# Performance work log

Hardware: AMD Instinct MI355X
Metric: run time of the kernel (lower is better)

The kernel has to match this reference:

```python
import jax, jax.numpy as jnp
import numpy as np

B, L, D, H, NL, V, W = 4, 2048, 512, 8, 4, 258, 8
HD = D // H


def setup_inputs() -> dict:
    key = jax.random.key(0)
    ks = jax.random.split(key, 12)
    s = 0.02
    x = jax.random.randint(ks[0], (B, L), 0, V, dtype=jnp.int32)
    patch_lengths = jnp.full((B, 256), W, dtype=jnp.int32)  # sum over patches == L
    emb = jax.random.normal(ks[1], (V, D), jnp.float32) * s
    ent_w = jax.random.normal(ks[2], (D, 1), jnp.float32) * s
    ent_b = jnp.zeros((D,), jnp.float32)
    qkv_w = jax.random.normal(ks[3], (NL, 3 * D, D), jnp.float32) * s
    qkv_b = jnp.zeros((NL, 3 * D), jnp.float32)
    ao_w = jax.random.normal(ks[4], (NL, D, D), jnp.float32) * s
    ao_b = jnp.zeros((NL, D), jnp.float32)
    ln1_s = jnp.ones((NL, D), jnp.float32)
    ln1_b = jnp.zeros((NL, D), jnp.float32)
    ln2_s = jnp.ones((NL, D), jnp.float32)
    ln2_b = jnp.zeros((NL, D), jnp.float32)
    ff1_w = jax.random.normal(ks[5], (NL, 4 * D, D), jnp.float32) * s
    ff1_b = jnp.zeros((NL, 4 * D), jnp.float32)
    ff2_w = jax.random.normal(ks[6], (NL, D, 4 * D), jnp.float32) * s
    ff2_b = jnp.zeros((NL, D), jnp.float32)
    out_w = jax.random.normal(ks[7], (V, D), jnp.float32) * s
    return {"emb": emb, "ent_w": ent_w, "ent_b": ent_b, "qkv_w": qkv_w,
            "qkv_b": qkv_b, "ao_w": ao_w, "ao_b": ao_b, "ln1_s": ln1_s,
            "ln1_b": ln1_b, "ln2_s": ln2_s, "ln2_b": ln2_b, "ff1_w": ff1_w,
            "ff1_b": ff1_b, "ff2_w": ff2_w, "ff2_b": ff2_b, "out_w": out_w,
            "x": x, "patch_lengths": patch_lengths}


def _layernorm(h, scale, bias, eps=1e-5):
    mu = jnp.mean(h, axis=-1, keepdims=True)
    var = jnp.mean(jnp.square(h - mu), axis=-1, keepdims=True)
    return (h - mu) * jax.lax.rsqrt(var + eps) * scale + bias


def _entropy_features(x, dtype):
    # fused sliding-window histogram via one-hot cumsum (replaces per-window bincount loop)
    onehot = jax.nn.one_hot(x, 256, dtype=dtype)            # [B, L, 256]
    c = jnp.cumsum(onehot, axis=1)
    cpad = jnp.concatenate([jnp.zeros_like(c[:, :1]), c], axis=1)
    counts = cpad[:, W:] - cpad[:, :-W]                     # [B, L-W+1, 256]
    p = counts / W
    ent = -jnp.sum(p * jnp.log2(p + 1e-10), axis=-1)        # zero-count terms contribute exactly 0
    full = jnp.zeros(x.shape, dtype).at[:, :x.shape[1] - W + 1].set(ent)
    return full[..., None]                                  # [B, L, 1]


def _block(h, p):
    qkv_w, qkv_b, ao_w, ao_b, l1s, l1b, l2s, l2b, f1w, f1b, f2w, f2b = p
    g = _layernorm(h, l1s, l1b)
    qkv = g @ qkv_w.T + qkv_b                                # [B, L, 3D]
    q, k, v = jnp.split(qkv, 3, axis=-1)
    q = q.reshape(B, L, H, HD)
    k = k.reshape(B, L, H, HD)
    v = v.reshape(B, L, H, HD)
    scores = jnp.einsum('blhd,bmhd->bhlm', q, k) / np.sqrt(HD).astype(h.dtype)
    attn = jax.nn.softmax(scores, axis=-1)
    o = jnp.einsum('bhlm,bmhd->blhd', attn, v).reshape(B, L, D)
    h = h + o @ ao_w.T + ao_b
    g = _layernorm(h, l2s, l2b)
    g = jax.nn.gelu(g @ f1w.T + f1b, approximate=False) @ f2w.T + f2b
    return h + g, None


def reference(emb, ent_w, ent_b, qkv_w, qkv_b, ao_w, ao_b, ln1_s, ln1_b,
              ln2_s, ln2_b, ff1_w, ff1_b, ff2_w, ff2_b, out_w, x, patch_lengths):
    tok = emb[x]                                             # [B, L, D]
    ent = _entropy_features(x, tok.dtype)                    # [B, L, 1]
    ent_emb = ent * ent_w[:, 0] + ent_b                      # Linear(1, D)
    h = tok + ent_emb
    h, _ = jax.lax.scan(_block, h,
                        (qkv_w, qkv_b, ao_w, ao_b, ln1_s, ln1_b,
                         ln2_s, ln2_b, ff1_w, ff1_b, ff2_w, ff2_b))
    # NOTE: the original module's global_transformer/patch-pool branch does not
    # feed the returned logits (dead code); logits come from the local stream h.
    logits = h @ out_w.T                                     # [B, L, V]
    return logits
```

## Files before the change

### kernel.cpp

```cpp
#include <hip/hip_runtime.h>
#include <hip/hip_bf16.h>
#include <math.h>

#define BB 4
#define LL 2048
#define DD 512
#define HH 8
#define NLAYER 4
#define VV 258
#define WW 8
#define HDIM 64
#define MM (BB * LL)
#define VPAD 384

#define C8 0.18033688f

typedef __attribute__((ext_vector_type(8))) short short8v;
typedef __attribute__((ext_vector_type(4))) float float4v;

typedef __attribute__((address_space(3))) unsigned int lds_u32;
typedef const __attribute__((address_space(1))) unsigned int glb_u32;

__device__ __forceinline__ unsigned short f2bf(float x) {
    unsigned int u = __float_as_uint(x);
    unsigned int r = (u + 0x7fffu + ((u >> 16) & 1u)) >> 16;
    return (unsigned short)r;
}
__device__ __forceinline__ float bf2f(unsigned short u) {
    return __uint_as_float((unsigned)u << 16);
}

__device__ __forceinline__ unsigned lds_addr(const void* p) {
    return (unsigned)(size_t)(__attribute__((address_space(3))) const void*)p;
}

#define E0 (NLAYER * 3 * DD * DD)
#define E1 (E0 + NLAYER * DD * DD)
#define E2 (E1 + NLAYER * 4 * DD * DD)
#define E3 (E2 + NLAYER * 4 * DD * DD)
#define E4 (E3 + VPAD * DD)

__global__ __launch_bounds__(256)
void cvt_all_kernel(const float* __restrict__ qkv_w, const float* __restrict__ ao_w,
                    const float* __restrict__ ff1_w, const float* __restrict__ ff2_w,
                    const float* __restrict__ out_w, unsigned short* __restrict__ dst)
{
    int i = (blockIdx.x * 256 + threadIdx.x) * 4;
    float4 v;
    if (i < E0)      v = *reinterpret_cast<const float4*>(qkv_w + i);
    else if (i < E1) v = *reinterpret_cast<const float4*>(ao_w + (i - E0));
    else if (i < E2) v = *reinterpret_cast<const float4*>(ff1_w + (i - E1));
    else if (i < E3) v = *reinterpret_cast<const float4*>(ff2_w + (i - E2));
    else {
        int idx = i - E3;
        if ((idx >> 9) < VV) v = *reinterpret_cast<const float4*>(out_w + idx);
        else                 v = (float4){0.f, 0.f, 0.f, 0.f};
    }
    uint2 pk;
    pk.x = (unsigned)f2bf(v.x) | ((unsigned)f2bf(v.y) << 16);
    pk.y = (unsigned)f2bf(v.z) | ((unsigned)f2bf(v.w) << 16);
    *reinterpret_cast<uint2*>(dst + i) = pk;
}

__global__ __launch_bounds__(256)
void embed_ln_kernel(const int* __restrict__ x,
                     const float* __restrict__ emb,
                     const float* __restrict__ ent_w,
                     const float* __restrict__ ent_b,
                     const float* __restrict__ ln_s,
                     const float* __restrict__ ln_b,
                     unsigned short* __restrict__ h,
                     unsigned short* __restrict__ g)
{
    int w = threadIdx.x >> 6, lane = threadIdx.x & 63;
    int row = blockIdx.x * 4 + w;
    int b = row / LL, l = row % LL;

    float ent = 0.f;
    if (l <= LL - WW) {
        int win[WW];
        #pragma unroll
        for (int i = 0; i < WW; i++) win[i] = x[b * LL + l + i];
        float s = 0.f;
        #pragma unroll
        for (int i = 0; i < WW; i++) {
            if (win[i] < 256) {
                int c = 0;
                #pragma unroll
                for (int j = 0; j < WW; j++) c += (win[j] == win[i]) ? 1 : 0;
                s += log2f((float)c * 0.125f + 1e-10f);
            }
        }
        ent = -s * 0.125f;
    }

    int tok = x[row];
    const float* erow = emb + (size_t)tok * DD + lane * 8;
    float v[8], ew[8], eb[8];
    *reinterpret_cast<float4*>(v)      = *reinterpret_cast<const float4*>(erow);
    *reinterpret_cast<float4*>(v + 4)  = *reinterpret_cast<const float4*>(erow + 4);
    *reinterpret_cast<float4*>(ew)     = *reinterpret_cast<const float4*>(ent_w + lane * 8);
    *reinterpret_cast<float4*>(ew + 4) = *reinterpret_cast<const float4*>(ent_w + lane * 8 + 4);
    *reinterpret_cast<float4*>(eb)     = *reinterpret_cast<const float4*>(ent_b + lane * 8);
    *reinterpret_cast<float4*>(eb + 4) = *reinterpret_cast<const float4*>(ent_b + lane * 8 + 4);

    float sum = 0.f, sq = 0.f;
    #pragma unroll
    for (int i = 0; i < 8; i++) {
        v[i] = v[i] + ent * ew[i] + eb[i];
        sum += v[i]; sq += v[i] * v[i];
    }
    unsigned int hpk[4];
    #pragma unroll
    for (int i = 0; i < 4; i++)
        hpk[i] = (unsigned)f2bf(v[2*i]) | ((unsigned)f2bf(v[2*i+1]) << 16);
    *reinterpret_cast<uint4*>(h + (size_t)row * DD + lane * 8) =
        *reinterpret_cast<const uint4*>(hpk);

    #pragma unroll
    for (int off = 32; off > 0; off >>= 1) {
        sum += __shfl_xor(sum, off);
        sq  += __shfl_xor(sq, off);
    }
    float mu = sum * (1.f / DD);
    float var = sq * (1.f / DD) - mu * mu;
    float rstd = rsqrtf(var + 1e-5f);

    float s8[8], bi[8];
    *reinterpret_cast<float4*>(s8)     = *reinterpret_cast<const float4*>(ln_s + lane * 8);
    *reinterpret_cast<float4*>(s8 + 4) = *reinterpret_cast<const float4*>(ln_s + lane * 8 + 4);
    *reinterpret_cast<float4*>(bi)     = *reinterpret_cast<const float4*>(ln_b + lane * 8);
    *reinterpret_cast<float4*>(bi + 4) = *reinterpret_cast<const float4*>(ln_b + lane * 8 + 4);

    unsigned int pk[4];
    #pragma unroll
    for (int i = 0; i < 4; i++) {
        unsigned short lo = f2bf((v[2*i]   - mu) * rstd * s8[2*i]   + bi[2*i]);
        unsigned short hi = f2bf((v[2*i+1] - mu) * rstd * s8[2*i+1] + bi[2*i+1]);
        pk[i] = (unsigned)lo | ((unsigned)hi << 16);
    }
    *reinterpret_cast<uint4*>(g + (size_t)row * DD + lane * 8) =
        *reinterpret_cast<const uint4*>(pk);
}

__global__ __launch_bounds__(256)
void ln_kernel(const unsigned short* __restrict__ h,
               const float* __restrict__ scale,
               const float* __restrict__ bias,
               unsigned short* __restrict__ g)
{
    int w = threadIdx.x >> 6, lane = threadIdx.x & 63;
    int row = blockIdx.x * 4 + w;

    uint4 raw = *reinterpret_cast<const uint4*>(h + (size_t)row * DD + lane * 8);
    const unsigned* rw = reinterpret_cast<const unsigned*>(&raw);
    float v[8];
    #pragma unroll
    for (int i = 0; i < 4; i++) {
        v[2*i]   = __uint_as_float(rw[i] << 16);
        v[2*i+1] = __uint_as_float(rw[i] & 0xffff0000u);
    }

    float sum = 0.f, sq = 0.f;
    #pragma unroll
    for (int i = 0; i < 8; i++) { sum += v[i]; sq += v[i] * v[i]; }
    #pragma unroll
    for (int off = 32; off > 0; off >>= 1) {
        sum += __shfl_xor(sum, off);
        sq  += __shfl_xor(sq, off);
    }
    float mu = sum * (1.f / DD);
    float var = sq * (1.f / DD) - mu * mu;
    float rstd = rsqrtf(var + 1e-5f);

    float s[8], bi[8];
    *reinterpret_cast<float4*>(s)      = *reinterpret_cast<const float4*>(scale + lane * 8);
    *reinterpret_cast<float4*>(s + 4)  = *reinterpret_cast<const float4*>(scale + lane * 8 + 4);
    *reinterpret_cast<float4*>(bi)     = *reinterpret_cast<const float4*>(bias + lane * 8);
    *reinterpret_cast<float4*>(bi + 4) = *reinterpret_cast<const float4*>(bias + lane * 8 + 4);

    unsigned int pk[4];
    #pragma unroll
    for (int i = 0; i < 4; i++) {
        unsigned short lo = f2bf((v[2*i]   - mu) * rstd * s[2*i]   + bi[2*i]);
        unsigned short hi = f2bf((v[2*i+1] - mu) * rstd * s[2*i+1] + bi[2*i+1]);
        pk[i] = (unsigned)lo | ((unsigned)hi << 16);
    }
    *reinterpret_cast<uint4*>(g + (size_t)row * DD + lane * 8) =
        *reinterpret_cast<const uint4*>(pk);
}

template<bool HAS_BIAS, bool GELU, bool RESID, bool QSCALE, int OMODE, int MT>
__global__ __launch_bounds__(MT * 2)
void gemm_mfma(const unsigned short* __restrict__ A,
               const unsigned short* __restrict__ W,
               const float* __restrict__ bias,
               const unsigned short* __restrict__ resid,
               void* __restrict__ Cv,
               int Nn, int Kk)
{
    constexpr int NW = MT / 32;
    constexpr int BLOADS = 512 / MT;
    constexpr int VMN = 4 + BLOADS;

    __shared__ unsigned short As[2][MT * 64];
    __shared__ unsigned short Bs[2][128 * 64];

    int t = threadIdx.x;
    int w = t >> 6, lane = t & 63;
    int wr = (MT == 128) ? (w >> 1) : 0;
    int wc = (MT == 128) ? (w & 1) : w;
    int l15 = lane & 15, l4 = lane >> 4;
    int m0 = blockIdx.y * MT, n0 = blockIdx.x * 128;

    int lrow = lane >> 3;
    int segp = (lane & 7) ^ lrow;

    float4v acc[4][4];
    #pragma unroll
    for (int i = 0; i < 4; i++)
        #pragma unroll
        for (int j = 0; j < 4; j++)
            acc[i][j] = (float4v){0.f, 0.f, 0.f, 0.f};

    #define STAGE(buf, k0) do {                                                   \
        _Pragma("unroll")                                                         \
        for (int i_ = 0; i_ < 4; i_++) {                                          \
            int r_ = i_ * (NW * 8) + w * 8 + lrow;                                \
            __builtin_amdgcn_global_load_lds(                                     \
                (glb_u32*)(A + (size_t)(m0 + r_) * Kk + (k0) + segp * 8),         \
                (lds_u32*)(As[buf] + i_ * (NW * 512) + w * 512), 16, 0, 0);       \
        }                                                                         \
        _Pragma("unroll")                                                         \
        for (int i_ = 0; i_ < BLOADS; i_++) {                                     \
            int r_ = i_ * (NW * 8) + w * 8 + lrow;                                \
            __builtin_amdgcn_global_load_lds(                                     \
                (glb_u32*)(W + (size_t)(n0 + r_) * Kk + (k0) + segp * 8),         \
                (lds_u32*)(Bs[buf] + i_ * (NW * 512) + w * 512), 16, 0, 0);       \
        } } while (0)

    int nk = Kk >> 6;
    STAGE(0, 0);
    for (int kt = 0; kt < nk; kt++) {
        int cur = kt & 1;
        if (kt + 1 < nk) {
            STAGE(cur ^ 1, (kt + 1) << 6);
            __builtin_amdgcn_sched_barrier(0);
            if constexpr (VMN == 8)  asm volatile("s_waitcnt vmcnt(8)");
            else                     asm volatile("s_waitcnt vmcnt(12)");
            __builtin_amdgcn_sched_barrier(0);
        } else {
            __builtin_amdgcn_sched_barrier(0);
            asm volatile("s_waitcnt vmcnt(0)");
            __builtin_amdgcn_sched_barrier(0);
        }
        __builtin_amdgcn_s_barrier();

        const char* asb = (const char*)As[cur];
        const char* bsb = (const char*)Bs[cur];
        #pragma unroll
        for (int kc = 0; kc < 2; kc++) {
            short8v af[4], bfr[4];
            #pragma unroll
            for (int mf = 0; mf < 4; mf++) {
                int row = wr * 64 + mf * 16 + l15;
                int off = (row * 128 + kc * 64 + l4 * 16) ^ ((row & 7) << 4);
                af[mf] = *reinterpret_cast<const short8v*>(asb + off);
            }
            #pragma unroll
            for (int nf = 0; nf < 4; nf++) {
                int row = wc * 64 + nf * 16 + l15;
                int off = (row * 128 + kc * 64 + l4 * 16) ^ ((row & 7) << 4);
                bfr[nf] = *reinterpret_cast<const short8v*>(bsb + off);
            }
            #pragma unroll
            for (int mf = 0; mf < 4; mf++)
                #pragma unroll
                for (int nf = 0; nf < 4; nf++)
                    acc[mf][nf] = __builtin_amdgcn_mfma_f32_16x16x32_bf16(
                        af[mf], bfr[nf], acc[mf][nf], 0, 0, 0);
        }
        __builtin_amdgcn_s_barrier();
    }
    #undef STAGE

    #pragma unroll
    for (int mf = 0; mf < 4; mf++)
        #pragma unroll
        for (int nf = 0; nf < 4; nf++)
            #pragma unroll
            for (int r = 0; r < 4; r++) {
                int m = m0 + wr * 64 + mf * 16 + l4 * 4 + r;
                int n = n0 + wc * 64 + nf * 16 + l15;
                if (n < Nn) {
                    float v = acc[mf][nf][r];
                    if (HAS_BIAS) v += bias[n];
                    if (GELU) {
                        float a = 0.044715f * v * v;
                        float u = fminf(fmaf(a, v, v) * 2.3022077f, 80.f);
                        float e = __builtin_amdgcn_exp2f(u);
                        v = v * e * __builtin_amdgcn_rcpf(e + 1.f);
                    }
                    if (RESID)    v += bf2f(resid[(size_t)m * Nn + n]);
                    if (QSCALE && n < DD) v *= C8;
                    if (OMODE == 1)
                        ((unsigned short*)Cv)[(size_t)m * Nn + n] = f2bf(v);
                    else
                        ((float*)Cv)[(size_t)m * Nn + n] = v;
                }
            }
}

__global__ __launch_bounds__(512, 2)
void attn_mfma(const unsigned short* __restrict__ qkv, unsigned short* __restrict__ o)
{
    __shared__ unsigned short Kl[2][128 * 64];
    __shared__ unsigned short Vs[2][128 * 64];
    __shared__ float Scl[8][16];

    int t = threadIdx.x, w = t >> 6, lane = t & 63;
    int l15 = lane & 15, l4 = lane >> 4;

    int flat = blockIdx.x;
    int swz = (flat & 7) * 64 + (flat >> 3);
    int qt = swz & 15, hh = (swz >> 4) & 7, b = swz >> 7;

    int q0 = qt * 128 + w * 16;
    const int RS = 3 * DD;

    short8v qf[2];
    #pragma unroll
    for (int dh = 0; dh < 2; dh++) {
        size_t addr = (size_t)(b * LL + q0 + l15) * RS + hh * HDIM + dh * 32 + l4 * 8;
        qf[dh] = *reinterpret_cast<const short8v*>(qkv + addr);
    }

    float4v o_acc[4];
    #pragma unroll
    for (int dt = 0; dt < 4; dt++) o_acc[dt] = (float4v){0.f, 0.f, 0.f, 0.f};
    float l_run = 0.f;

    int lrow8 = lane >> 3;
    int ksegp = (lane & 7) ^ lrow8;
    int rho = w * 8 + lrow8;
    int kappa = ((rho >> 5) << 5) | (((rho >> 4) & 1) << 2)
              | (((rho >> 2) & 3) << 3) | (rho & 3);
    int vrow = ((t >> 5) << 2) | ((t >> 1) & 3);
    int vseg = (((t >> 3) & 3) << 1) | (t & 1);
    const unsigned short* kgl = qkv + (size_t)(b * LL + kappa) * RS
                              + hh * HDIM + DD + ksegp * 8;
    const unsigned short* vgl = qkv + (size_t)(b * LL + vrow) * RS
                              + hh * HDIM + 2 * DD + vseg * 8;
    const int halfstep = 64 * RS;
    const int step = 128 * RS;

    #define ASTAGE(buf) do {                                                      \
        __builtin_amdgcn_global_load_lds((glb_u32*)kgl,                           \
            (lds_u32*)(Kl[buf] + w * 512), 16, 0, 0);                             \
        __builtin_amdgcn_global_load_lds((glb_u32*)(kgl + halfstep),              \
            (lds_u32*)(Kl[buf] + 4096 + w * 512), 16, 0, 0);                      \
        __builtin_amdgcn_global_load_lds((glb_u32*)vgl,                           \
            (lds_u32*)(Vs[buf] + w * 512), 16, 0, 0);                             \
        __builtin_amdgcn_global_load_lds((glb_u32*)(vgl + halfstep),              \
            (lds_u32*)(Vs[buf] + 4096 + w * 512), 16, 0, 0);                      \
        kgl += step; vgl += step; } while (0)

    unsigned vtrbase = lds_addr(Vs) + ((lane >> 4) << 10)
                     + (((lane >> 2) & 3) << 5) + ((lane & 3) << 3);

    ASTAGE(0);
    asm volatile("s_waitcnt vmcnt(0)");
    __syncthreads();

    for (int kb = 0; kb < LL / 128; kb++) {
        int cur = kb & 1;
        if (kb + 1 < LL / 128) ASTAGE(cur ^ 1);

        #pragma unroll
        for (int hf = 0; hf < 2; hf++) {
            const char* klc = (const char*)Kl[cur] + hf * 8192;
            unsigned vb = vtrbase + cur * 16384 + hf * 8192;

            float4v s_acc[4];
            __builtin_amdgcn_s_setprio(1);
            #pragma unroll
            for (int nt = 0; nt < 4; nt++) {
                s_acc[nt] = (float4v){0.f, 0.f, 0.f, 0.f};
                #pragma unroll
                for (int dh = 0; dh < 2; dh++) {
                    int row = nt * 16 + l15;
                    int off = (row * 128 + dh * 64 + l4 * 16) ^ ((row & 7) << 4);
                    short8v kf = *reinterpret_cast<const short8v*>(klc + off);
                    s_acc[nt] = __builtin_amdgcn_mfma_f32_16x16x32_bf16(kf, qf[dh], s_acc[nt], 0, 0, 0);
                }
            }
            __builtin_amdgcn_s_setprio(0);

            unsigned long long a0, a1, a2, a3, a4, a5, a6, a7;
            unsigned long long b0, b1, b2, b3, b4, b5, b6, b7;
            unsigned ab0 = vb, ab1 = vb + 4096;
            asm volatile("ds_read_b64_tr_b16 %0, %1" : "=v"(a0) : "v"(ab0));
            asm volatile("ds_read_b64_tr_b16 %0, %1" : "=v"(a1) : "v"(ab0 + 512));
            asm volatile("ds_read_b64_tr_b16 %0, %1" : "=v"(a2) : "v"(ab0 + 128));
            asm volatile("ds_read_b64_tr_b16 %0, %1" : "=v"(a3) : "v"(ab0 + 640));
            asm volatile("ds_read_b64_tr_b16 %0, %1" : "=v"(a4) : "v"(ab0 + 256));
            asm volatile("ds_read_b64_tr_b16 %0, %1" : "=v"(a5) : "v"(ab0 + 768));
            asm volatile("ds_read_b64_tr_b16 %0, %1" : "=v"(a6) : "v"(ab0 + 384));
            asm volatile("ds_read_b64_tr_b16 %0, %1" : "=v"(a7) : "v"(ab0 + 896));
            asm volatile("ds_read_b64_tr_b16 %0, %1" : "=v"(b0) : "v"(ab1));
            asm volatile("ds_read_b64_tr_b16 %0, %1" : "=v"(b1) : "v"(ab1 + 512));
            asm volatile("ds_read_b64_tr_b16 %0, %1" : "=v"(b2) : "v"(ab1 + 128));
            asm volatile("ds_read_b64_tr_b16 %0, %1" : "=v"(b3) : "v"(ab1 + 640));
            asm volatile("ds_read_b64_tr_b16 %0, %1" : "=v"(b4) : "v"(ab1 + 256));
            asm volatile("ds_read_b64_tr_b16 %0, %1" : "=v"(b5) : "v"(ab1 + 768));
            asm volatile("ds_read_b64_tr_b16 %0, %1" : "=v"(b6) : "v"(ab1 + 384));
            asm volatile("ds_read_b64_tr_b16 %0, %1" : "=v"(b7) : "v"(ab1 + 896));

            union { unsigned u[4]; short8v v; } pf0u, pf1u;
            float ps;
            {
                float p0 = __builtin_amdgcn_exp2f(s_acc[0][0]);
                float p1 = __builtin_amdgcn_exp2f(s_acc[0][1]);
                float p2 = __builtin_amdgcn_exp2f(s_acc[0][2]);
                float p3 = __builtin_amdgcn_exp2f(s_acc[0][3]);
                float p4 = __builtin_amdgcn_exp2f(s_acc[1][0]);
                float p5 = __builtin_amdgcn_exp2f(s_acc[1][1]);
                float p6 = __builtin_amdgcn_exp2f(s_acc[1][2]);
                float p7 = __builtin_amdgcn_exp2f(s_acc[1][3]);
                asm("v_cvt_pk_bf16_f32 %0, %1, %2" : "=v"(pf0u.u[0]) : "v"(p0), "v"(p1));
                asm("v_cvt_pk_bf16_f32 %0, %1, %2" : "=v"(pf0u.u[1]) : "v"(p2), "v"(p3));
                asm("v_cvt_pk_bf16_f32 %0, %1, %2" : "=v"(pf0u.u[2]) : "v"(p4), "v"(p5));
                asm("v_cvt_pk_bf16_f32 %0, %1, %2" : "=v"(pf0u.u[3]) : "v"(p6), "v"(p7));
                ps = ((p0 + p1) + (p2 + p3)) + ((p4 + p5) + (p6 + p7));
            }
            {
                float p0 = __builtin_amdgcn_exp2f(s_acc[2][0]);
                float p1 = __builtin_amdgcn_exp2f(s_acc[2][1]);
                float p2 = __builtin_amdgcn_exp2f(s_acc[2][2]);
                float p3 = __builtin_amdgcn_exp2f(s_acc[2][3]);
                float p4 = __builtin_amdgcn_exp2f(s_acc[3][0]);
                float p5 = __builtin_amdgcn_exp2f(s_acc[3][1]);
                float p6 = __builtin_amdgcn_exp2f(s_acc[3][2]);
                float p7 = __builtin_amdgcn_exp2f(s_acc[3][3]);
                asm("v_cvt_pk_bf16_f32 %0, %1, %2" : "=v"(pf1u.u[0]) : "v"(p0), "v"(p1));
                asm("v_cvt_pk_bf16_f32 %0, %1, %2" : "=v"(pf1u.u[1]) : "v"(p2), "v"(p3));
                asm("v_cvt_pk_bf16_f32 %0, %1, %2" : "=v"(pf1u.u[2]) : "v"(p4), "v"(p5));
                asm("v_cvt_pk_bf16_f32 %0, %1, %2" : "=v"(pf1u.u[3]) : "v"(p6), "v"(p7));
                ps += ((p0 + p1) + (p2 + p3)) + ((p4 + p5) + (p6 + p7));
            }
            l_run += ps;

            union { unsigned long long q[2]; short8v v; } u0, u1, u2, u3;
            asm volatile("s_waitcnt lgkmcnt(8)");
            __builtin_amdgcn_sched_barrier(0);
            __builtin_amdgcn_s_setprio(1);
            u0.q[0] = a0; u0.q[1] = a1;
            u1.q[0] = a2; u1.q[1] = a3;
            o_acc[0] = __builtin_amdgcn_mfma_f32_16x16x32_bf16(pf0u.v, u0.v, o_acc[0], 0, 0, 0);
            o_acc[1] = __builtin_amdgcn_mfma_f32_16x16x32_bf16(pf0u.v, u1.v, o_acc[1], 0, 0, 0);
            asm volatile("s_waitcnt lgkmcnt(4)");
            __builtin_amdgcn_sched_barrier(0);
            u2.q[0] = a4; u2.q[1] = a5;
            u3.q[0] = a6; u3.q[1] = a7;
            o_acc[2] = __builtin_amdgcn_mfma_f32_16x16x32_bf16(pf0u.v, u2.v, o_acc[2], 0, 0, 0);
            o_acc[3] = __builtin_amdgcn_mfma_f32_16x16x32_bf16(pf0u.v, u3.v, o_acc[3], 0, 0, 0);
            asm volatile("s_waitcnt lgkmcnt(0)");
            __builtin_amdgcn_sched_barrier(0);
            u0.q[0] = b0; u0.q[1] = b1;
            u1.q[0] = b2; u1.q[1] = b3;
            u2.q[0] = b4; u2.q[1] = b5;
            u3.q[0] = b6; u3.q[1] = b7;
            o_acc[0] = __builtin_amdgcn_mfma_f32_16x16x32_bf16(pf1u.v, u0.v, o_acc[0], 0, 0, 0);
            o_acc[1] = __builtin_amdgcn_mfma_f32_16x16x32_bf16(pf1u.v, u1.v, o_acc[1], 0, 0, 0);
            o_acc[2] = __builtin_amdgcn_mfma_f32_16x16x32_bf16(pf1u.v, u2.v, o_acc[2], 0, 0, 0);
            o_acc[3] = __builtin_amdgcn_mfma_f32_16x16x32_bf16(pf1u.v, u3.v, o_acc[3], 0, 0, 0);
            __builtin_amdgcn_s_setprio(0);
        }

        asm volatile("s_waitcnt vmcnt(0)");
        __syncthreads();
    }
    #undef ASTAGE

    float lt = l_run;
    lt += __shfl_xor(lt, 16);
    lt += __shfl_xor(lt, 32);
    if (l4 == 0) Scl[w][l15] = 1.f / lt;
    float4 iv = *reinterpret_cast<const float4*>(&Scl[w][l4 * 4]);
    float invs[4] = {iv.x, iv.y, iv.z, iv.w};
    #pragma unroll
    for (int r = 0; r < 4; r++) {
        int qg = q0 + l4 * 4 + r;
        #pragma unroll
        for (int dt = 0; dt < 4; dt++) {
            o[(size_t)(b * LL + qg) * DD + hh * HDIM + dt * 16 + l15] =
                f2bf(o_acc[dt][r] * invs[r]);
        }
    }
}

extern "C" void kernel_launch(void* const* d_in, const int* in_sizes, int n_in,
                              void* d_out, int out_size, void* d_ws, size_t ws_size,
                              hipStream_t stream)
{
    const float* emb    = (const float*)d_in[0];
    const float* ent_w  = (const float*)d_in[1];
    const float* ent_b  = (const float*)d_in[2];
    const float* qkv_w  = (const float*)d_in[3];
    const float* qkv_b  = (const float*)d_in[4];
    const float* ao_w   = (const float*)d_in[5];
    const float* ao_b   = (const float*)d_in[6];
    const float* ln1_s  = (const float*)d_in[7];
    const float* ln1_b  = (const float*)d_in[8];
    const float* ln2_s  = (const float*)d_in[9];
    const float* ln2_b  = (const float*)d_in[10];
    const float* ff1_w  = (const float*)d_in[11];
    const float* ff1_b  = (const float*)d_in[12];
    const float* ff2_w  = (const float*)d_in[13];
    const float* ff2_b  = (const float*)d_in[14];
    const float* out_w  = (const float*)d_in[15];
    const int*   x      = (const int*)d_in[16];

    float* out = (float*)d_out;

    const int NQW = NLAYER * 3 * DD * DD;
    const int NAW = NLAYER * DD * DD;
    const int NF1 = NLAYER * 4 * DD * DD;
    const int NF2 = NLAYER * DD * 4 * DD;

    char* p = (char*)d_ws;
    unsigned short* wq  = (unsigned short*)p; p += (size_t)NQW * 2;
    unsigned short* wa  = (unsigned short*)p; p += (size_t)NAW * 2;
    unsigned short* w1  = (unsigned short*)p; p += (size_t)NF1 * 2;
    unsigned short* w2  = (unsigned short*)p; p += (size_t)NF2 * 2;
    unsigned short* wob = (unsigned short*)p; p += (size_t)VPAD * DD * 2;
    unsigned short* h   = (unsigned short*)p; p += (size_t)MM * DD * 2;
    unsigned short* gb  = (unsigned short*)p; p += (size_t)MM * DD * 2;
    unsigned short* ob  = (unsigned short*)p; p += (size_t)MM * DD * 2;
    unsigned short* bb  = (unsigned short*)p; p += (size_t)MM * 4 * DD * 2;

    dim3 blk(256);

    cvt_all_kernel<<<E4 / 1024, blk, 0, stream>>>(qkv_w, ao_w, ff1_w, ff2_w, out_w, wq);

    embed_ln_kernel<<<MM / 4, blk, 0, stream>>>(x, emb, ent_w, ent_b,
                                                ln1_s, ln1_b, h, gb);

    for (int layer = 0; layer < NLAYER; layer++) {
        const unsigned short* qw = wq + (size_t)layer * 3 * DD * DD;
        const unsigned short* aw = wa + (size_t)layer * DD * DD;
        const unsigned short* f1 = w1 + (size_t)layer * 4 * DD * DD;
        const unsigned short* f2 = w2 + (size_t)layer * DD * 4 * DD;
        const float* qb  = qkv_b + (size_t)layer * 3 * DD;
        const float* ab  = ao_b  + (size_t)layer * DD;
        const float* l1s = ln1_s + (size_t)layer * DD;
        const float* l1b = ln1_b + (size_t)layer * DD;
        const float* l2s = ln2_s + (size_t)layer * DD;
        const float* l2b = ln2_b + (size_t)layer * DD;
        const float* f1b = ff1_b + (size_t)layer * 4 * DD;
        const float* f2b = ff2_b + (size_t)layer * DD;

        if (layer > 0)
            ln_kernel<<<MM / 4, blk, 0, stream>>>(h, l1s, l1b, gb);

        {
            dim3 grid((3 * DD) / 128, MM / 128);
            gemm_mfma<true, false, false, true, 1, 128><<<grid, 256, 0, stream>>>(
                gb, qw, qb, nullptr, bb, 3 * DD, DD);
        }

        attn_mfma<<<512, 512, 0, stream>>>(bb, ob);

        {
            dim3 grid(DD / 128, MM / 64);
            gemm_mfma<true, false, true, false, 1, 64><<<grid, 128, 0, stream>>>(
                ob, aw, ab, h, h, DD, DD);
        }

        ln_kernel<<<MM / 4, blk, 0, stream>>>(h, l2s, l2b, gb);

        {
            dim3 grid((4 * DD) / 128, MM / 128);
            gemm_mfma<true, true, false, false, 1, 128><<<grid, 256, 0, stream>>>(
                gb, f1, f1b, nullptr, bb, 4 * DD, DD);
        }

        {
            dim3 grid(DD / 128, MM / 64);
            gemm_mfma<true, false, true, false, 1, 64><<<grid, 128, 0, stream>>>(
                bb, f2, f2b, h, h, DD, 4 * DD);
        }
    }

    {
        dim3 grid(VPAD / 128, MM / 64);
        gemm_mfma<false, false, false, false, 0, 64><<<grid, 128, 0, stream>>>(
            h, wob, nullptr, nullptr, out, VV, DD);
    }
}
```

Before: 702.0 us.

## Process two query tiles per wave in attention to reuse K/V fragments

Each wave now handles 32 query rows as two independent 16-row tiles, sharing every K fragment and V transpose read between them. The grid halves to 256 blocks of 256 queries. This amortizes LDS reads and global K/V staging over twice as much MFMA work and gives independent MFMA chains. In exchange it doubles accumulator registers and halves the number of blocks, which may reduce occupancy and latency hiding.

```diff
diff --git a/kernel.cpp b/kernel.cpp
--- a/kernel.cpp
+++ b/kernel.cpp
@@ -316,29 +316,33 @@
 {
     __shared__ unsigned short Kl[2][128 * 64];
     __shared__ unsigned short Vs[2][128 * 64];
-    __shared__ float Scl[8][16];
+    __shared__ float Scl[8][2][16];
 
     int t = threadIdx.x, w = t >> 6, lane = t & 63;
     int l15 = lane & 15, l4 = lane >> 4;
 
     int flat = blockIdx.x;
-    int swz = (flat & 7) * 64 + (flat >> 3);
-    int qt = swz & 15, hh = (swz >> 4) & 7, b = swz >> 7;
-
-    int q0 = qt * 128 + w * 16;
+    int swz = (flat & 7) * 32 + (flat >> 3);
+    int qt = swz & 7, hh = (swz >> 3) & 7, b = swz >> 6;
+
+    int q0 = qt * 256 + w * 32;
     const int RS = 3 * DD;
 
-    short8v qf[2];
+    short8v qfA[2], qfB[2];
     #pragma unroll
     for (int dh = 0; dh < 2; dh++) {
-        size_t addr = (size_t)(b * LL + q0 + l15) * RS + hh * HDIM + dh * 32 + l4 * 8;
-        qf[dh] = *reinterpret_cast<const short8v*>(qkv + addr);
-    }
-
-    float4v o_acc[4];
-    #pragma unroll
-    for (int dt = 0; dt < 4; dt++) o_acc[dt] = (float4v){0.f, 0.f, 0.f, 0.f};
-    float l_run = 0.f;
+        size_t addrA = (size_t)(b * LL + q0 + l15) * RS + hh * HDIM + dh * 32 + l4 * 8;
+        qfA[dh] = *reinterpret_cast<const short8v*>(qkv + addrA);
+        qfB[dh] = *reinterpret_cast<const short8v*>(qkv + addrA + 16 * RS);
+    }
+
+    float4v oA[4], oB[4];
+    #pragma unroll
+    for (int dt = 0; dt < 4; dt++) {
+        oA[dt] = (float4v){0.f, 0.f, 0.f, 0.f};
+        oB[dt] = (float4v){0.f, 0.f, 0.f, 0.f};
+    }
+    float lA = 0.f, lB = 0.f;
 
     int lrow8 = lane >> 3;
     int ksegp = (lane & 7) ^ lrow8;
@@ -381,17 +385,19 @@
             const char* klc = (const char*)Kl[cur] + hf * 8192;
             unsigned vb = vtrbase + cur * 16384 + hf * 8192;
 
-            float4v s_acc[4];
+            float4v sA[4], sB[4];
             __builtin_amdgcn_s_setprio(1);
             #pragma unroll
             for (int nt = 0; nt < 4; nt++) {
-                s_acc[nt] = (float4v){0.f, 0.f, 0.f, 0.f};
+                sA[nt] = (float4v){0.f, 0.f, 0.f, 0.f};
+                sB[nt] = (float4v){0.f, 0.f, 0.f, 0.f};
                 #pragma unroll
                 for (int dh = 0; dh < 2; dh++) {
                     int row = nt * 16 + l15;
                     int off = (row * 128 + dh * 64 + l4 * 16) ^ ((row & 7) << 4);
                     short8v kf = *reinterpret_cast<const short8v*>(klc + off);
-                    s_acc[nt] = __builtin_amdgcn_mfma_f32_16x16x32_bf16(kf, qf[dh], s_acc[nt], 0, 0, 0);
+                    sA[nt] = __builtin_amdgcn_mfma_f32_16x16x32_bf16(kf, qfA[dh], sA[nt], 0, 0, 0);
+                    sB[nt] = __builtin_amdgcn_mfma_f32_16x16x32_bf16(kf, qfB[dh], sB[nt], 0, 0, 0);
                 }
             }
             __builtin_amdgcn_s_setprio(0);
@@ -416,39 +422,63 @@
             asm volatile("ds_read_b64_tr_b16 %0, %1" : "=v"(b6) : "v"(ab1 + 384));
             asm volatile("ds_read_b64_tr_b16 %0, %1" : "=v"(b7) : "v"(ab1 + 896));
 
-            union { unsigned u[4]; short8v v; } pf0u, pf1u;
-            float ps;
+            union { unsigned u[4]; short8v v; } pf0A, pf1A, pf0B, pf1B;
             {
-                float p0 = __builtin_amdgcn_exp2f(s_acc[0][0]);
-                float p1 = __builtin_amdgcn_exp2f(s_acc[0][1]);
-                float p2 = __builtin_amdgcn_exp2f(s_acc[0][2]);
-                float p3 = __builtin_amdgcn_exp2f(s_acc[0][3]);
-                float p4 = __builtin_amdgcn_exp2f(s_acc[1][0]);
-                float p5 = __builtin_amdgcn_exp2f(s_acc[1][1]);
-                float p6 = __builtin_amdgcn_exp2f(s_acc[1][2]);
-                float p7 = __builtin_amdgcn_exp2f(s_acc[1][3]);
-                asm("v_cvt_pk_bf16_f32 %0, %1, %2" : "=v"(pf0u.u[0]) : "v"(p0), "v"(p1));
-                asm("v_cvt_pk_bf16_f32 %0, %1, %2" : "=v"(pf0u.u[1]) : "v"(p2), "v"(p3));
-                asm("v_cvt_pk_bf16_f32 %0, %1, %2" : "=v"(pf0u.u[2]) : "v"(p4), "v"(p5));
-                asm("v_cvt_pk_bf16_f32 %0, %1, %2" : "=v"(pf0u.u[3]) : "v"(p6), "v"(p7));
-                ps = ((p0 + p1) + (p2 + p3)) + ((p4 + p5) + (p6 + p7));
+                float p0 = __builtin_amdgcn_exp2f(sA[0][0]);
+                float p1 = __builtin_amdgcn_exp2f(sA[0][1]);
+                float p2 = __builtin_amdgcn_exp2f(sA[0][2]);
+                float p3 = __builtin_amdgcn_exp2f(sA[0][3]);
+                float p4 = __builtin_amdgcn_exp2f(sA[1][0]);
+                float p5 = __builtin_amdgcn_exp2f(sA[1][1]);
+                float p6 = __builtin_amdgcn_exp2f(sA[1][2]);
+                float p7 = __builtin_amdgcn_exp2f(sA[1][3]);
+                asm("v_cvt_pk_bf16_f32 %0, %1, %2" : "=v"(pf0A.u[0]) : "v"(p0), "v"(p1));
+                asm("v_cvt_pk_bf16_f32 %0, %1, %2" : "=v"(pf0A.u[1]) : "v"(p2), "v"(p3));
+                asm("v_cvt_pk_bf16_f32 %0, %1, %2" : "=v"(pf0A.u[2]) : "v"(p4), "v"(p5));
+                asm("v_cvt_pk_bf16_f32 %0, %1, %2" : "=v"(pf0A.u[3]) : "v"(p6), "v"(p7));
+                float q0_ = __builtin_amdgcn_exp2f(sA[2][0]);
+                float q1_ = __builtin_amdgcn_exp2f(sA[2][1]);
+                float q2_ = __builtin_amdgcn_exp2f(sA[2][2]);
+                float q3_ = __builtin_amdgcn_exp2f(sA[2][3]);
+                float q4_ = __builtin_amdgcn_exp2f(sA[3][0]);
+                float q5_ = __builtin_amdgcn_exp2f(sA[3][1]);
+                float q6_ = __builtin_amdgcn_exp2f(sA[3][2]);
+                float q7_ = __builtin_amdgcn_exp2f(sA[3][3]);
+                asm("v_cvt_pk_bf16_f32 %0, %1, %2" : "=v"(pf1A.u[0]) : "v"(q0_), "v"(q1_));
+                asm("v_cvt_pk_bf16_f32 %0, %1, %2" : "=v"(pf1A.u[1]) : "v"(q2_), "v"(q3_));
+                asm("v_cvt_pk_bf16_f32 %0, %1, %2" : "=v"(pf1A.u[2]) : "v"(q4_), "v"(q5_));
+                asm("v_cvt_pk_bf16_f32 %0, %1, %2" : "=v"(pf1A.u[3]) : "v"(q6_), "v"(q7_));
+                lA += ((p0 + p1) + (p2 + p3)) + ((p4 + p5) + (p6 + p7))
+                    + ((q0_ + q1_) + (q2_ + q3_)) + ((q4_ + q5_) + (q6_ + q7_));
             }
             {
-                float p0 = __builtin_amdgcn_exp2f(s_acc[2][0]);
-                float p1 = __builtin_amdgcn_exp2f(s_acc[2][1]);
-                float p2 = __builtin_amdgcn_exp2f(s_acc[2][2]);
-                float p3 = __builtin_amdgcn_exp2f(s_acc[2][3]);
-                float p4 = __builtin_amdgcn_exp2f(s_acc[3][0]);
-                float p5 = __builtin_amdgcn_exp2f(s_acc[3][1]);
-                float p6 = __builtin_amdgcn_exp2f(s_acc[3][2]);
-                float p7 = __builtin_amdgcn_exp2f(s_acc[3][3]);
-                asm("v_cvt_pk_bf16_f32 %0, %1, %2" : "=v"(pf1u.u[0]) : "v"(p0), "v"(p1));
-                asm("v_cvt_pk_bf16_f32 %0, %1, %2" : "=v"(pf1u.u[1]) : "v"(p2), "v"(p3));
-                asm("v_cvt_pk_bf16_f32 %0, %1, %2" : "=v"(pf1u.u[2]) : "v"(p4), "v"(p5));
-                asm("v_cvt_pk_bf16_f32 %0, %1, %2" : "=v"(pf1u.u[3]) : "v"(p6), "v"(p7));
-                ps += ((p0 + p1) + (p2 + p3)) + ((p4 + p5) + (p6 + p7));
+                float p0 = __builtin_amdgcn_exp2f(sB[0][0]);
+                float p1 = __builtin_amdgcn_exp2f(sB[0][1]);
+                float p2 = __builtin_amdgcn_exp2f(sB[0][2]);
+                float p3 = __builtin_amdgcn_exp2f(sB[0][3]);
+                float p4 = __builtin_amdgcn_exp2f(sB[1][0]);
+                float p5 = __builtin_amdgcn_exp2f(sB[1][1]);
+                float p6 = __builtin_amdgcn_exp2f(sB[1][2]);
+                float p7 = __builtin_amdgcn_exp2f(sB[1][3]);
+                asm("v_cvt_pk_bf16_f32 %0, %1, %2" : "=v"(pf0B.u[0]) : "v"(p0), "v"(p1));
+                asm("v_cvt_pk_bf16_f32 %0, %1, %2" : "=v"(pf0B.u[1]) : "v"(p2), "v"(p3));
+                asm("v_cvt_pk_bf16_f32 %0, %1, %2" : "=v"(pf0B.u[2]) : "v"(p4), "v"(p5));
+                asm("v_cvt_pk_bf16_f32 %0, %1, %2" : "=v"(pf0B.u[3]) : "v"(p6), "v"(p7));
+                float q0_ = __builtin_amdgcn_exp2f(sB[2][0]);
+                float q1_ = __builtin_amdgcn_exp2f(sB[2][1]);
+                float q2_ = __builtin_amdgcn_exp2f(sB[2][2]);
+                float q3_ = __builtin_amdgcn_exp2f(sB[2][3]);
+                float q4_ = __builtin_amdgcn_exp2f(sB[3][0]);
+                float q5_ = __builtin_amdgcn_exp2f(sB[3][1]);
+                float q6_ = __builtin_amdgcn_exp2f(sB[3][2]);
+                float q7_ = __builtin_amdgcn_exp2f(sB[3][3]);
+                asm("v_cvt_pk_bf16_f32 %0, %1, %2" : "=v"(pf1B.u[0]) : "v"(q0_), "v"(q1_));
+                asm("v_cvt_pk_bf16_f32 %0, %1, %2" : "=v"(pf1B.u[1]) : "v"(q2_), "v"(q3_));
+                asm("v_cvt_pk_bf16_f32 %0, %1, %2" : "=v"(pf1B.u[2]) : "v"(q4_), "v"(q5_));
+                asm("v_cvt_pk_bf16_f32 %0, %1, %2" : "=v"(pf1B.u[3]) : "v"(q6_), "v"(q7_));
+                lB += ((p0 + p1) + (p2 + p3)) + ((p4 + p5) + (p6 + p7))
+                    + ((q0_ + q1_) + (q2_ + q3_)) + ((q4_ + q5_) + (q6_ + q7_));
             }
-            l_run += ps;
 
             union { unsigned long long q[2]; short8v v; } u0, u1, u2, u3;
             asm volatile("s_waitcnt lgkmcnt(8)");
@@ -456,24 +486,32 @@
             __builtin_amdgcn_s_setprio(1);
             u0.q[0] = a0; u0.q[1] = a1;
             u1.q[0] = a2; u1.q[1] = a3;
-            o_acc[0] = __builtin_amdgcn_mfma_f32_16x16x32_bf16(pf0u.v, u0.v, o_acc[0], 0, 0, 0);
-            o_acc[1] = __builtin_amdgcn_mfma_f32_16x16x32_bf16(pf0u.v, u1.v, o_acc[1], 0, 0, 0);
+            oA[0] = __builtin_amdgcn_mfma_f32_16x16x32_bf16(pf0A.v, u0.v, oA[0], 0, 0, 0);
+            oB[0] = __builtin_amdgcn_mfma_f32_16x16x32_bf16(pf0B.v, u0.v, oB[0], 0, 0, 0);
+            oA[1] = __builtin_amdgcn_mfma_f32_16x16x32_bf16(pf0A.v, u1.v, oA[1], 0, 0, 0);
+            oB[1] = __builtin_amdgcn_mfma_f32_16x16x32_bf16(pf0B.v, u1.v, oB[1], 0, 0, 0);
             asm volatile("s_waitcnt lgkmcnt(4)");
             __builtin_amdgcn_sched_barrier(0);
             u2.q[0] = a4; u2.q[1] = a5;
             u3.q[0] = a6; u3.q[1] = a7;
-            o_acc[2] = __builtin_amdgcn_mfma_f32_16x16x32_bf16(pf0u.v, u2.v, o_acc[2], 0, 0, 0);
-            o_acc[3] = __builtin_amdgcn_mfma_f32_16x16x32_bf16(pf0u.v, u3.v, o_acc[3], 0, 0, 0);
+            oA[2] = __builtin_amdgcn_mfma_f32_16x16x32_bf16(pf0A.v, u2.v, oA[2], 0, 0, 0);
+            oB[2] = __builtin_amdgcn_mfma_f32_16x16x32_bf16(pf0B.v, u2.v, oB[2], 0, 0, 0);
+            oA[3] = __builtin_amdgcn_mfma_f32_16x16x32_bf16(pf0A.v, u3.v, oA[3], 0, 0, 0);
+            oB[3] = __builtin_amdgcn_mfma_f32_16x16x32_bf16(pf0B.v, u3.v, oB[3], 0, 0, 0);
             asm volatile("s_waitcnt lgkmcnt(0)");
             __builtin_amdgcn_sched_barrier(0);
             u0.q[0] = b0; u0.q[1] = b1;
             u1.q[0] = b2; u1.q[1] = b3;
             u2.q[0] = b4; u2.q[1] = b5;
             u3.q[0] = b6; u3.q[1] = b7;
-            o_acc[0] = __builtin_amdgcn_mfma_f32_16x16x32_bf16(pf1u.v, u0.v, o_acc[0], 0, 0, 0);
-            o_acc[1] = __builtin_amdgcn_mfma_f32_16x16x32_bf16(pf1u.v, u1.v, o_acc[1], 0, 0, 0);
-            o_acc[2] = __builtin_amdgcn_mfma_f32_16x16x32_bf16(pf1u.v, u2.v, o_acc[2], 0, 0, 0);
-            o_acc[3] = __builtin_amdgcn_mfma_f32_16x16x32_bf16(pf1u.v, u3.v, o_acc[3], 0, 0, 0);
+            oA[0] = __builtin_amdgcn_mfma_f32_16x16x32_bf16(pf1A.v, u0.v, oA[0], 0, 0, 0);
+            oB[0] = __builtin_amdgcn_mfma_f32_16x16x32_bf16(pf1B.v, u0.v, oB[0], 0, 0, 0);
+            oA[1] = __builtin_amdgcn_mfma_f32_16x16x32_bf16(pf1A.v, u1.v, oA[1], 0, 0, 0);
+            oB[1] = __builtin_amdgcn_mfma_f32_16x16x32_bf16(pf1B.v, u1.v, oB[1], 0, 0, 0);
+            oA[2] = __builtin_amdgcn_mfma_f32_16x16x32_bf16(pf1A.v, u2.v, oA[2], 0, 0, 0);
+            oB[2] = __builtin_amdgcn_mfma_f32_16x16x32_bf16(pf1B.v, u2.v, oB[2], 0, 0, 0);
+            oA[3] = __builtin_amdgcn_mfma_f32_16x16x32_bf16(pf1A.v, u3.v, oA[3], 0, 0, 0);
+            oB[3] = __builtin_amdgcn_mfma_f32_16x16x32_bf16(pf1B.v, u3.v, oB[3], 0, 0, 0);
             __builtin_amdgcn_s_setprio(0);
         }
 
@@ -482,19 +520,23 @@
     }
     #undef ASTAGE
 
-    float lt = l_run;
-    lt += __shfl_xor(lt, 16);
-    lt += __shfl_xor(lt, 32);
-    if (l4 == 0) Scl[w][l15] = 1.f / lt;
-    float4 iv = *reinterpret_cast<const float4*>(&Scl[w][l4 * 4]);
-    float invs[4] = {iv.x, iv.y, iv.z, iv.w};
+    float ltA = lA, ltB = lB;
+    ltA += __shfl_xor(ltA, 16); ltA += __shfl_xor(ltA, 32);
+    ltB += __shfl_xor(ltB, 16); ltB += __shfl_xor(ltB, 32);
+    if (l4 == 0) { Scl[w][0][l15] = 1.f / ltA; Scl[w][1][l15] = 1.f / ltB; }
+    float4 ivA = *reinterpret_cast<const float4*>(&Scl[w][0][l4 * 4]);
+    float4 ivB = *reinterpret_cast<const float4*>(&Scl[w][1][l4 * 4]);
+    float invA[4] = {ivA.x, ivA.y, ivA.z, ivA.w};
+    float invB[4] = {ivB.x, ivB.y, ivB.z, ivB.w};
     #pragma unroll
     for (int r = 0; r < 4; r++) {
-        int qg = q0 + l4 * 4 + r;
+        int qgA = q0 + l4 * 4 + r;
         #pragma unroll
         for (int dt = 0; dt < 4; dt++) {
-            o[(size_t)(b * LL + qg) * DD + hh * HDIM + dt * 16 + l15] =
-                f2bf(o_acc[dt][r] * invs[r]);
+            o[(size_t)(b * LL + qgA) * DD + hh * HDIM + dt * 16 + l15] =
+                f2bf(oA[dt][r] * invA[r]);
+            o[(size_t)(b * LL + qgA + 16) * DD + hh * HDIM + dt * 16 + l15] =
+                f2bf(oB[dt][r] * invB[r]);
         }
     }
 }
@@ -569,7 +611,7 @@
                 gb, qw, qb, nullptr, bb, 3 * DD, DD);
         }
 
-        attn_mfma<<<512, 512, 0, stream>>>(bb, ob);
+        attn_mfma<<<256, 512, 0, stream>>>(bb, ob);
 
         {
             dim3 grid(DD / 128, MM / 64);
```

After: 720.6 us. +2.7%, slower.
